# Optimization experiments

Measured on AMD Instinct MI355X. Metric: run time of the kernel, lower is better.

The kernel has to match this reference:

```python
import jax, jax.numpy as jnp
import numpy as np

B, S, VOCAB, E, H, T = 256, 512, 50000, 256, 256, 32
PAD = VOCAB - 1  # mask = sentences != vocab_size - 1 in the original


def setup_inputs() -> dict:
    key = jax.random.key(0)
    ks = jax.random.split(key, 16)
    lengths = jnp.sort(jax.random.randint(ks[0], (B,), S // 2, S + 1))[::-1]
    lengths = lengths.at[0].set(S)  # sorted descending, max length present
    sentences = jax.random.randint(ks[1], (B, S), 0, VOCAB - 1)
    pos = jnp.arange(S)
    sentences = jnp.where(pos[None, :] < lengths[:, None], sentences, PAD)
    tags = jax.random.randint(ks[2], (B, S), 0, T)
    sc = jnp.float32(0.1)
    p = lambda k, shp: jax.random.normal(k, shp, jnp.float32) * sc
    return {
        'embed_table': p(ks[3], (VOCAB + 1, E)),
        'W_ih_f': p(ks[4], (4 * H, E)), 'W_hh_f': p(ks[5], (4 * H, H)),
        'b_ih_f': p(ks[6], (4 * H,)), 'b_hh_f': p(ks[7], (4 * H,)),
        'W_ih_b': p(ks[8], (4 * H, E)), 'W_hh_b': p(ks[9], (4 * H, H)),
        'b_ih_b': p(ks[10], (4 * H,)), 'b_hh_b': p(ks[11], (4 * H,)),
        'W_out': p(ks[12], (T, 2 * H)), 'b_out': p(ks[13], (T,)),
        'transition': jax.random.normal(ks[14], (T, T), jnp.float32),
        'sentences': sentences, 'tags': tags, 'sen_lengths': lengths,
    }


def _run_lstm(x_sbe, W_ih, W_hh, b_ih, b_hh):
    # x_sbe: [S, B, E]; torch gate order i, f, g, o
    Bsz, Hd = x_sbe.shape[1], W_hh.shape[1]
    gx = jnp.einsum('sbe,ge->sbg', x_sbe, W_ih) + b_ih + b_hh  # precompute input gates
    def step(carry, g):
        h, c = carry
        g = g + h @ W_hh.T
        i, f, gg, o = jnp.split(g, 4, axis=-1)
        c = jax.nn.sigmoid(f) * c + jax.nn.sigmoid(i) * jnp.tanh(gg)
        h = jax.nn.sigmoid(o) * jnp.tanh(c)
        return (h, c), h
    h0 = jnp.zeros((Bsz, Hd), x_sbe.dtype)
    _, hs = jax.lax.scan(step, (h0, h0), gx)
    return hs  # [S, B, H]


def _forward(embed_table, W_ih_f, W_hh_f, b_ih_f, b_hh_f,
             W_ih_b, W_hh_b, b_ih_b, b_hh_b, W_out, b_out, transition,
             sentences, tags, sen_lengths):
    mask = sentences != PAD                      # [B, S]
    x = embed_table[sentences]                   # [B, S, E]
    pos = jnp.arange(S)
    valid = pos[None, :] < sen_lengths[:, None]  # [B, S]
    # per-sequence reversal index (packed-sequence-faithful backward direction)
    idx = jnp.where(valid, sen_lengths[:, None] - 1 - pos[None, :], pos[None, :])
    h_f = _run_lstm(x.transpose(1, 0, 2), W_ih_f, W_hh_f, b_ih_f, b_hh_f).transpose(1, 0, 2)
    x_rev = jnp.take_along_axis(x, idx[:, :, None], axis=1)
    h_b = _run_lstm(x_rev.transpose(1, 0, 2), W_ih_b, W_hh_b, b_ih_b, b_hh_b).transpose(1, 0, 2)
    h_b = jnp.take_along_axis(h_b, idx[:, :, None], axis=1)
    h = jnp.concatenate([h_f, h_b], -1) * valid[:, :, None]  # pad_packed pads with zeros
    emit = h @ W_out.T + b_out                   # [B, S, T]; dropout is identity (eval)
    # ---- CRF negative log-likelihood ----
    fmask = mask.astype(emit.dtype)
    real = jnp.take_along_axis(emit, tags[:, :, None], axis=2)[..., 0]  # [B, S]
    real = real.at[:, 1:].add(transition[tags[:, :-1], tags[:, 1:]])
    real_score = (real * fmask).sum(axis=1)      # [B]
    def crf_step(alpha, inp):
        e_i, m_i = inp                           # [B, T], [B]
        scores = alpha[:, :, None] + transition[None, :, :] + e_i[:, None, :]
        new = jax.nn.logsumexp(scores, axis=1)
        return jnp.where(m_i[:, None], new, alpha), None
    alpha0 = emit[:, 0]                          # [B, T]
    xs = (emit[:, 1:].transpose(1, 0, 2), mask[:, 1:].T)
    alpha, _ = jax.lax.scan(crf_step, alpha0, xs)
    log_z = jax.nn.logsumexp(alpha, axis=1)      # [B]
    return -(real_score - log_z)                 # per-example loss [B]


def reference(embed_table, W_ih_f, W_hh_f, b_ih_f, b_hh_f,
              W_ih_b, W_hh_b, b_ih_b, b_hh_b, W_out, b_out, transition,
              sentences, tags, sen_lengths):
    return _forward(embed_table, W_ih_f, W_hh_f, b_ih_f, b_hh_f,
                    W_ih_b, W_hh_b, b_ih_b, b_hh_b, W_out, b_out, transition,
                    sentences, tags, sen_lengths)
```

## Files before the change

kernel.cpp:

```cpp
#include <hip/hip_runtime.h>
#include <hip/hip_bf16.h>


typedef __bf16 bf16x8 __attribute__((ext_vector_type(8)));
typedef float f32x4 __attribute__((ext_vector_type(4)));
typedef unsigned int uint4v __attribute__((ext_vector_type(4)));

__device__ __forceinline__ unsigned short f2bf(float f) {
  union { float f; unsigned int u; } v; v.f = f;
  unsigned int r = v.u + 0x7fffu + ((v.u >> 16) & 1u);
  return (unsigned short)(r >> 16);
}
__device__ __forceinline__ float bf2f(unsigned int lo16) {
  union { unsigned int u; float f; } v; v.u = lo16 << 16;
  return v.f;
}
__device__ __forceinline__ float fsig(float x) {
  float e = __builtin_amdgcn_exp2f(-1.4426950408889634f * x);
  return __builtin_amdgcn_rcpf(1.0f + e);
}
__device__ __forceinline__ float ftanh(float x) {
  float e = __builtin_amdgcn_exp2f(2.8853900817779268f * x);
  return 1.0f - 2.0f * __builtin_amdgcn_rcpf(e + 1.0f);
}

__global__ void cvt_weights(const float* __restrict__ wih_f, const float* __restrict__ wih_b,
                            const float* __restrict__ whh_f, const float* __restrict__ whh_b,
                            const float* __restrict__ wo,
                            unsigned short* __restrict__ wih,
                            unsigned char* __restrict__ whh8,
                            unsigned char* __restrict__ wout8) {
  int t = blockIdx.x * 256 + threadIdx.x;
  int i = t * 4;
  if (i < 524288) {
    const float* src = (i < 262144) ? wih_f : wih_b;
    f32x4 v = *(const f32x4*)(src + (i & 262143));
    uint2 p;
    p.x = f2bf(v[0]) | ((unsigned int)f2bf(v[1]) << 16);
    p.y = f2bf(v[2]) | ((unsigned int)f2bf(v[3]) << 16);
    *(uint2*)(wih + i) = p;
  } else if (i < 1048576) {
    int k = i - 524288;
    const float* src = (k < 262144) ? whh_f : whh_b;
    f32x4 v = *(const f32x4*)(src + (k & 262143));
    int r = 0;
    r = __builtin_amdgcn_cvt_pk_fp8_f32(v[0], v[1], r, false);
    r = __builtin_amdgcn_cvt_pk_fp8_f32(v[2], v[3], r, true);
    *(unsigned int*)(whh8 + k) = (unsigned int)r;
  } else if (i < 1064960) {
    int k = i - 1048576;
    f32x4 v = *(const f32x4*)(wo + k);
    int r = 0;
    r = __builtin_amdgcn_cvt_pk_fp8_f32(v[0], v[1], r, false);
    r = __builtin_amdgcn_cvt_pk_fp8_f32(v[2], v[3], r, true);
    *(unsigned int*)(wout8 + k) = (unsigned int)r;
  }
}


__device__ __forceinline__ void gemm_role(
    const float* __restrict__ emb, const int* __restrict__ sent, const int* __restrict__ lens,
    const unsigned short* __restrict__ wih,
    const float* __restrict__ bih_f, const float* __restrict__ bhh_f,
    const float* __restrict__ bih_b, const float* __restrict__ bhh_b,
    unsigned short* __restrict__ gx, int k,
    unsigned short* wtile, float* btile)
{
  int g = blockIdx.x - 64;
  int dir = g >> 7, r = g & 127;
  int nc = r >> 4, bt = (r >> 2) & 3, ss = r & 3;
  int n0 = nc * 128, bbase = bt * 64;
  int s0 = k * 32;
  int sbase = s0 + ss * 8;
  if (sbase >= lens[bbase]) return;
  int p = k & 1;
  int tid = threadIdx.x, w = tid >> 6, lane = tid & 63, col = lane & 15, q = lane >> 4;
  int ns = w >> 2, cg = w & 3;

  const unsigned short* wsrc = wih + (size_t)dir * 262144;
#pragma unroll
  for (int it = 0; it < 8; it++) {
    int seg = it * 512 + tid;
    int row = seg >> 5, kc = (seg & 31) * 8;
    *(uint4v*)(wtile + row * 264 + kc) = *(const uint4v*)(wsrc + (size_t)(n0 + row) * 256 + kc);
  }
  const float* bi = dir ? bih_b : bih_f;
  const float* bh = dir ? bhh_b : bhh_f;
  if (tid < 128) btile[tid] = bi[n0 + tid] + bh[n0 + tid];
  __syncthreads();

  bf16x8 wf[8][4];
#pragma unroll
  for (int kt = 0; kt < 8; kt++)
#pragma unroll
    for (int nt = 0; nt < 4; nt++)
      wf[kt][nt] = *(const bf16x8*)(wtile + (ns * 64 + nt * 16 + col) * 264 + kt * 32 + q * 8);
  f32x4 bias[4];
#pragma unroll
  for (int nt = 0; nt < 4; nt++)
#pragma unroll
    for (int rr = 0; rr < 4; rr++)
      bias[nt][rr] = btile[ns * 64 + nt * 16 + q * 4 + rr];

  int bidx = bbase + cg * 16 + col;
  int len = lens[bidx];
  const int* srow = sent + bidx * 512;

  for (int i = 0; i < 8; i++) {
    int s = sbase + i;
    int s_eff = dir ? ((s < len) ? (len - 1 - s) : s) : s;
    int token = srow[s_eff];
    const float* ep = emb + (size_t)token * 256;
    bf16x8 xf[8];
#pragma unroll
    for (int kt = 0; kt < 8; kt++) {
      f32x4 a0 = *(const f32x4*)(ep + kt * 32 + q * 8);
      f32x4 a1 = *(const f32x4*)(ep + kt * 32 + q * 8 + 4);
      uint4v pk;
      pk[0] = f2bf(a0[0]) | ((unsigned int)f2bf(a0[1]) << 16);
      pk[1] = f2bf(a0[2]) | ((unsigned int)f2bf(a0[3]) << 16);
      pk[2] = f2bf(a1[0]) | ((unsigned int)f2bf(a1[1]) << 16);
      pk[3] = f2bf(a1[2]) | ((unsigned int)f2bf(a1[3]) << 16);
      xf[kt] = __builtin_bit_cast(bf16x8, pk);
    }
    f32x4 acc[4];
#pragma unroll
    for (int nt = 0; nt < 4; nt++) acc[nt] = bias[nt];
#pragma unroll
    for (int kt = 0; kt < 8; kt++)
#pragma unroll
      for (int nt = 0; nt < 4; nt++)
        acc[nt] = __builtin_amdgcn_mfma_f32_16x16x32_bf16(wf[kt][nt], xf[kt], acc[nt], 0, 0, 0);
    size_t off = (size_t)p * 16777216 + (size_t)dir * 8388608
               + (size_t)(s - s0) * 262144 + (size_t)bidx * 1024 + n0 + ns * 64;
#pragma unroll
    for (int nt = 0; nt < 4; nt++) {
      uint2 pk;
      pk.x = f2bf(acc[nt][0]) | ((unsigned int)f2bf(acc[nt][1]) << 16);
      pk.y = f2bf(acc[nt][2]) | ((unsigned int)f2bf(acc[nt][3]) << 16);
      *(uint2*)(gx + off + nt * 16 + q * 4) = pk;
    }
  }
}

__device__ __forceinline__ void lstm_role(
    const unsigned short* __restrict__ gx,
    const unsigned char* __restrict__ whh8,
    const unsigned char* __restrict__ wout8,
    const float* __restrict__ bout,
    const int* __restrict__ lens,
    unsigned short* __restrict__ emit_f, unsigned short* __restrict__ emit_b,
    unsigned short* __restrict__ h_state, float* __restrict__ c_state,
    int k, unsigned char (*hbuf)[16 * 264])
{
  int cl = k - 1;
  int s0 = cl * 32, first = (cl == 0), p = cl & 1;
  int bx = blockIdx.x;
  int dir = bx & 1, grp = bx >> 1, b0 = grp * 8;
  int tid = threadIdx.x, w = tid >> 6, lane = tid & 63, col = lane & 15, q = lane >> 4;
  int maxlen = lens[b0];
  if (s0 >= maxlen) return;
  int send = s0 + 32; if (send > maxlen) send = maxlen;
  int bcl = b0 + col; if (bcl > 255) bcl = 255;
  int mylen = lens[bcl];

  const unsigned char* whb = whh8 + (size_t)dir * 262144;
  long wh[8][8];
#pragma unroll
  for (int kt = 0; kt < 8; kt++)
#pragma unroll
    for (int t = 0; t < 8; t++) {
      int row0 = (t & 3) * 256 + w * 32 + (t >> 2) * 16;
      wh[kt][t] = *(const long*)(whb + (size_t)(row0 + col) * 256 + kt * 32 + q * 8);
    }

  long wo8[8];
  f32x4 bo4 = (f32x4){0.f, 0.f, 0.f, 0.f};
  if (w < 2) {
#pragma unroll
    for (int kt = 0; kt < 8; kt++)
      wo8[kt] = *(const long*)(wout8 + (size_t)(w * 16 + col) * 512 + dir * 256 + kt * 32 + q * 8);
    if (dir == 0) {
#pragma unroll
      for (int r = 0; r < 4; r++) bo4[r] = bout[w * 16 + q * 4 + r];
    }
  }
  unsigned short* ebase = dir ? emit_b : emit_f;

  size_t stoff = ((size_t)bx * 16 + col) * 256 + w * 32;
  float c8[8];
  long hf8[8];
  if (first) {
#pragma unroll
    for (int i = 0; i < 8; i++) c8[i] = 0.f;
#pragma unroll
    for (int i = 0; i < 8; i++) hf8[i] = 0;
  } else {
    int pf = (s0 + 1) & 1;
#pragma unroll
    for (int a = 0; a < 2; a++) {
      f32x4 cv = *(const f32x4*)(c_state + stoff + a * 16 + q * 4);
#pragma unroll
      for (int r = 0; r < 4; r++) c8[a * 4 + r] = cv[r];
      uint2 hb = *(const uint2*)(h_state + stoff + a * 16 + q * 4);
      float h0 = bf2f(hb.x & 0xffffu), h1 = bf2f(hb.x >> 16);
      float h2 = bf2f(hb.y & 0xffffu), h3 = bf2f(hb.y >> 16);
      int r8 = 0;
      r8 = __builtin_amdgcn_cvt_pk_fp8_f32(h0, h1, r8, false);
      r8 = __builtin_amdgcn_cvt_pk_fp8_f32(h2, h3, r8, true);
      *(unsigned int*)(&hbuf[pf][col * 264 + w * 32 + a * 16 + q * 4]) = (unsigned int)r8;
    }
    __syncthreads();
#pragma unroll
    for (int kt = 0; kt < 8; kt++)
      hf8[kt] = *(const long*)(&hbuf[pf][col * 264 + kt * 32 + q * 8]);
  }

  const unsigned short* gl = gx + (size_t)p * 16777216 + (size_t)dir * 8388608
                                + (size_t)bcl * 1024 + q * 4;
  uint2 gxr[8];
#pragma unroll
  for (int t = 0; t < 8; t++) {
    int row0 = (t & 3) * 256 + w * 32 + (t >> 2) * 16;
    gxr[t] = *(const uint2*)(gl + row0);
  }

  for (int s = s0; s < send; s++) {
    f32x4 acc[8];
#pragma unroll
    for (int t = 0; t < 8; t++) {
      f32x4 a;
      a[0] = bf2f(gxr[t].x & 0xffffu); a[1] = bf2f(gxr[t].x >> 16);
      a[2] = bf2f(gxr[t].y & 0xffffu); a[3] = bf2f(gxr[t].y >> 16);
      acc[t] = a;
    }
    {
      int snl = (s + 1 < send) ? (s + 1 - s0) : (send - 1 - s0);
      const unsigned short* gn = gl + (size_t)snl * 262144;
#pragma unroll
      for (int t = 0; t < 8; t++) {
        int row0 = (t & 3) * 256 + w * 32 + (t >> 2) * 16;
        gxr[t] = *(const uint2*)(gn + row0);
      }
    }
#pragma unroll
    for (int kt = 0; kt < 8; kt++) {
      long hv8 = hf8[kt];
#pragma unroll
      for (int t = 0; t < 8; t++)
        acc[t] = __builtin_amdgcn_mfma_f32_16x16x32_fp8_fp8(wh[kt][t], hv8, acc[t], 0, 0, 0);
    }
    float hv[8];
#pragma unroll
    for (int a = 0; a < 2; a++)
#pragma unroll
      for (int r = 0; r < 4; r++) {
        float ig = acc[a * 4 + 0][r], fg = acc[a * 4 + 1][r];
        float gg = acc[a * 4 + 2][r], og = acc[a * 4 + 3][r];
        float cn = fsig(fg) * c8[a * 4 + r] + fsig(ig) * ftanh(gg);
        c8[a * 4 + r] = cn;
        hv[a * 4 + r] = fsig(og) * ftanh(cn);
      }
    int par = s & 1;
#pragma unroll
    for (int a = 0; a < 2; a++) {
      int r8 = 0;
      r8 = __builtin_amdgcn_cvt_pk_fp8_f32(hv[a * 4 + 0], hv[a * 4 + 1], r8, false);
      r8 = __builtin_amdgcn_cvt_pk_fp8_f32(hv[a * 4 + 2], hv[a * 4 + 3], r8, true);
      *(unsigned int*)(&hbuf[par][col * 264 + w * 32 + a * 16 + q * 4]) = (unsigned int)r8;
    }
    if (s == send - 1) {
#pragma unroll
      for (int a = 0; a < 2; a++) {
        uint2 pp;
        pp.x = f2bf(hv[a * 4 + 0]) | ((unsigned int)f2bf(hv[a * 4 + 1]) << 16);
        pp.y = f2bf(hv[a * 4 + 2]) | ((unsigned int)f2bf(hv[a * 4 + 3]) << 16);
        *(uint2*)(h_state + stoff + a * 16 + q * 4) = pp;
      }
    }
    __syncthreads();
#pragma unroll
    for (int kt = 0; kt < 8; kt++)
      hf8[kt] = *(const long*)(&hbuf[par][col * 264 + kt * 32 + q * 8]);

    if (w < 2) {
      f32x4 ea = bo4;
#pragma unroll
      for (int kt = 0; kt < 8; kt++)
        ea = __builtin_amdgcn_mfma_f32_16x16x32_fp8_fp8(wo8[kt], hf8[kt], ea, 0, 0, 0);
      if (col < 8 && s < mylen) {
        int pos = dir ? (mylen - 1 - s) : s;
        uint2 pk;
        pk.x = f2bf(ea[0]) | ((unsigned int)f2bf(ea[1]) << 16);
        pk.y = f2bf(ea[2]) | ((unsigned int)f2bf(ea[3]) << 16);
        *(uint2*)(ebase + (((size_t)(b0 + col) * 512 + pos) * 32 + w * 16 + q * 4)) = pk;
      }
    }
  }
#pragma unroll
  for (int a = 0; a < 2; a++) {
    f32x4 cv;
#pragma unroll
    for (int r = 0; r < 4; r++) cv[r] = c8[a * 4 + r];
    *(f32x4*)(c_state + stoff + a * 16 + q * 4) = cv;
  }
}

__global__ __launch_bounds__(512, 2) void fused_step(
    const float* __restrict__ emb, const int* __restrict__ sent, const int* __restrict__ lens,
    const unsigned short* __restrict__ wih,
    const float* __restrict__ bih_f, const float* __restrict__ bhh_f,
    const float* __restrict__ bih_b, const float* __restrict__ bhh_b,
    unsigned short* __restrict__ gx,
    const unsigned char* __restrict__ whh8, const unsigned char* __restrict__ wout8,
    const float* __restrict__ bout,
    unsigned short* __restrict__ emit_f, unsigned short* __restrict__ emit_b,
    unsigned short* __restrict__ h_state, float* __restrict__ c_state,
    int k)
{
  __shared__ __align__(16) unsigned short wtile[128 * 264];
  __shared__ __align__(16) float btile[128];
  __shared__ __align__(16) unsigned char hbuf[2][16 * 264];

  if (blockIdx.x < 64) {
    if (k == 0) return;
    lstm_role(gx, whh8, wout8, bout, lens, emit_f, emit_b, h_state, c_state, k, hbuf);
  } else {
    if (k == 16) return;
    gemm_role(emb, sent, lens, wih, bih_f, bhh_f, bih_b, bhh_b, gx, k, wtile, btile);
  }
}

__global__ __launch_bounds__(64) void crf_kernel(
    const unsigned short* __restrict__ emit_f,
    const unsigned short* __restrict__ emit_b,
    const float* __restrict__ trans, const int* __restrict__ tags,
    const int* __restrict__ lens, float* __restrict__ out) {
  const float LOG2E = 1.4426950408889634f, LN2 = 0.6931471805599453f;
  __shared__ __align__(16) float e_lds[512 * 32];
  int b = blockIdx.x, lane = threadIdx.x;
  int len = lens[b];
  const int* tg = tags + b * 512;

  size_t ebase = (size_t)b * 512 * 32;
  const unsigned short* pf = emit_f + ebase;
  const unsigned short* pb = emit_b + ebase;
  int ng = len * 4;
  for (int g = lane; g < ng; g += 64) {
    uint4v fv = *(const uint4v*)(pf + g * 8);
    uint4v bv = *(const uint4v*)(pb + g * 8);
    f32x4 w0, w1;
#pragma unroll
    for (int k = 0; k < 2; k++) {
      w0[2 * k]     = (bf2f(fv[k] & 0xffffu) + bf2f(bv[k] & 0xffffu)) * LOG2E;
      w0[2 * k + 1] = (bf2f(fv[k] >> 16)     + bf2f(bv[k] >> 16))     * LOG2E;
      w1[2 * k]     = (bf2f(fv[k + 2] & 0xffffu) + bf2f(bv[k + 2] & 0xffffu)) * LOG2E;
      w1[2 * k + 1] = (bf2f(fv[k + 2] >> 16)     + bf2f(bv[k + 2] >> 16))     * LOG2E;
    }
    *(f32x4*)(e_lds + g * 8) = w0;
    *(f32x4*)(e_lds + g * 8 + 4) = w1;
  }
  __syncthreads();

  float rs2 = 0.f, rst = 0.f;
  for (int s = lane; s < len; s += 64) {
    int t1 = tg[s];
    rs2 += e_lds[s * 32 + t1];
    if (s > 0) rst += trans[tg[s - 1] * 32 + t1];
  }
  float rsc = LN2 * rs2 + rst;
#pragma unroll
  for (int m = 32; m; m >>= 1) rsc += __shfl_xor(rsc, m);

  int j = lane & 31, half = lane >> 5, i0 = half * 16;
  float tr2[16];
  int pidx[16];
#pragma unroll
  for (int ii = 0; ii < 16; ii++) {
    tr2[ii] = trans[(i0 + ii) * 32 + j] * LOG2E;
    pidx[ii] = (i0 + ii) << 2;
  }
  const float* ep = e_lds + j;
  float B = ep[0];
  float e_nxt = ep[32];
  for (int s = 1; s < len; s++) {
    float e_cur = e_nxt;
    int sn = (s + 1 < len) ? (s + 1) : s;
    e_nxt = ep[sn * 32];
    float v[16];
#pragma unroll
    for (int ii = 0; ii < 16; ii++)
      v[ii] = __builtin_bit_cast(float, __builtin_amdgcn_ds_bpermute(
                  pidx[ii], __builtin_bit_cast(int, B))) + tr2[ii];
    float a8[8], a4[4], a2[2];
#pragma unroll
    for (int ii = 0; ii < 8; ii++) a8[ii] = fmaxf(v[ii], v[ii + 8]);
#pragma unroll
    for (int ii = 0; ii < 4; ii++) a4[ii] = fmaxf(a8[ii], a8[ii + 4]);
    a2[0] = fmaxf(a4[0], a4[2]); a2[1] = fmaxf(a4[1], a4[3]);
    float m1 = fmaxf(a2[0], a2[1]);
    float m2 = fmaxf(m1, __shfl_xor(m1, 32));
    float x[16];
#pragma unroll
    for (int ii = 0; ii < 16; ii++) x[ii] = __builtin_amdgcn_exp2f(v[ii] - m2);
    float s8[8], s4[4], s2[2];
#pragma unroll
    for (int ii = 0; ii < 8; ii++) s8[ii] = x[ii] + x[ii + 8];
#pragma unroll
    for (int ii = 0; ii < 4; ii++) s4[ii] = s8[ii] + s8[ii + 4];
    s2[0] = s4[0] + s4[2]; s2[1] = s4[1] + s4[3];
    float sum = s2[0] + s2[1];
    sum += __shfl_xor(sum, 32);
    B = m2 + __builtin_amdgcn_logf(sum) + e_cur;
  }
  float mz = B;
#pragma unroll
  for (int m = 16; m; m >>= 1) mz = fmaxf(mz, __shfl_xor(mz, m));
  float sz = __builtin_amdgcn_exp2f(B - mz);
#pragma unroll
  for (int m = 16; m; m >>= 1) sz += __shfl_xor(sz, m);
  float logz = LN2 * (mz + __builtin_amdgcn_logf(sz));
  if (lane == 0) out[b] = logz - rsc;
}

extern "C" void kernel_launch(void* const* d_in, const int* in_sizes, int n_in,
                              void* d_out, int out_size, void* d_ws, size_t ws_size,
                              hipStream_t stream) {
  const float* emb   = (const float*)d_in[0];
  const float* Wih_f = (const float*)d_in[1];
  const float* Whh_f = (const float*)d_in[2];
  const float* bih_f = (const float*)d_in[3];
  const float* bhh_f = (const float*)d_in[4];
  const float* Wih_b = (const float*)d_in[5];
  const float* Whh_b = (const float*)d_in[6];
  const float* bih_b = (const float*)d_in[7];
  const float* bhh_b = (const float*)d_in[8];
  const float* Wout  = (const float*)d_in[9];
  const float* bout  = (const float*)d_in[10];
  const float* trans = (const float*)d_in[11];
  const int* sent = (const int*)d_in[12];
  const int* tags = (const int*)d_in[13];
  const int* lens = (const int*)d_in[14];
  float* out = (float*)d_out;

  char* ws = (char*)d_ws;
  if (ws_size < 87048192ull) return;
  unsigned short* gx      = (unsigned short*)(ws);
  unsigned short* emit_f  = (unsigned short*)(ws + 67108864);
  unsigned short* emit_b  = (unsigned short*)(ws + 75497472);
  unsigned short* wih_bf  = (unsigned short*)(ws + 83886080);
  unsigned char*  whh8    = (unsigned char*)(ws + 84934656);
  unsigned char*  wout8   = (unsigned char*)(ws + 85458944);
  unsigned short* h_state = (unsigned short*)(ws + 85475328);
  float*          c_state = (float*)(ws + 85999616);

  cvt_weights<<<1040, 256, 0, stream>>>(Wih_f, Wih_b, Whh_f, Whh_b, Wout,
                                        wih_bf, whh8, wout8);
  for (int k = 0; k <= 16; k++) {
    fused_step<<<320, 512, 0, stream>>>(
        emb, sent, lens, wih_bf, bih_f, bhh_f, bih_b, bhh_b, gx,
        whh8, wout8, bout, emit_f, emit_b, h_state, c_state, k);
  }
  crf_kernel<<<256, 64, 0, stream>>>(emit_f, emit_b, trans, tags, lens, out);
}
```

Baseline: 1.665 ms.

## Replace per-chunk kernel launches with a persistent kernel using atomic flag handoff

Replaces the 17 sequential launches of the fused step with one persistent kernel. Its 64 LSTM blocks keep h and c in registers across all chunks, and 192 GEMM blocks loop over chunk tiles. Producer and consumer synchronise through release/acquire atomic counters in global memory. This removes per-launch overhead and the h/c state spill to global memory between chunks. It also lets the input-gate GEMM run ahead of the recurrence, limited by the double-buffered gx. The output projection is now batched every 4 steps from an 8-deep LDS h ring, using all warps. This adds a dependence on all 256 blocks being co-resident, otherwise the spin-waits could deadlock.

```diff
diff --git a/kernel.cpp b/kernel.cpp
--- a/kernel.cpp
+++ b/kernel.cpp
@@ -22,6 +22,15 @@
 __device__ __forceinline__ float ftanh(float x) {
   float e = __builtin_amdgcn_exp2f(2.8853900817779268f * x);
   return 1.0f - 2.0f * __builtin_amdgcn_rcpf(e + 1.0f);
+}
+
+__device__ __forceinline__ void wait_ge(int* p, int target) {
+  if (threadIdx.x == 0) {
+    while (__hip_atomic_load(p, __ATOMIC_RELAXED, __HIP_MEMORY_SCOPE_AGENT) < target)
+      __builtin_amdgcn_s_sleep(2);
+    (void)__hip_atomic_load(p, __ATOMIC_ACQUIRE, __HIP_MEMORY_SCOPE_AGENT);
+  }
+  __syncthreads();
 }
 
 __global__ void cvt_weights(const float* __restrict__ wih_f, const float* __restrict__ wih_b,
@@ -29,7 +38,9 @@
                             const float* __restrict__ wo,
                             unsigned short* __restrict__ wih,
                             unsigned char* __restrict__ whh8,
-                            unsigned char* __restrict__ wout8) {
+                            unsigned char* __restrict__ wout8,
+                            int* __restrict__ flags) {
+  if (blockIdx.x == 0 && threadIdx.x < 32) flags[threadIdx.x] = 0;
   int t = blockIdx.x * 256 + threadIdx.x;
   int i = t * 4;
   if (i < 524288) {
@@ -58,109 +69,115 @@
 }
 
 
-__device__ __forceinline__ void gemm_role(
+__device__ void gemm_role(
     const float* __restrict__ emb, const int* __restrict__ sent, const int* __restrict__ lens,
     const unsigned short* __restrict__ wih,
     const float* __restrict__ bih_f, const float* __restrict__ bhh_f,
     const float* __restrict__ bih_b, const float* __restrict__ bhh_b,
-    unsigned short* __restrict__ gx, int k,
+    unsigned short* __restrict__ gx, int* flags,
     unsigned short* wtile, float* btile)
 {
-  int g = blockIdx.x - 64;
-  int dir = g >> 7, r = g & 127;
-  int nc = r >> 4, bt = (r >> 2) & 3, ss = r & 3;
-  int n0 = nc * 128, bbase = bt * 64;
-  int s0 = k * 32;
-  int sbase = s0 + ss * 8;
-  if (sbase >= lens[bbase]) return;
-  int p = k & 1;
+  int gb = blockIdx.x - 64;
   int tid = threadIdx.x, w = tid >> 6, lane = tid & 63, col = lane & 15, q = lane >> 4;
   int ns = w >> 2, cg = w & 3;
-
-  const unsigned short* wsrc = wih + (size_t)dir * 262144;
-#pragma unroll
-  for (int it = 0; it < 8; it++) {
-    int seg = it * 512 + tid;
-    int row = seg >> 5, kc = (seg & 31) * 8;
-    *(uint4v*)(wtile + row * 264 + kc) = *(const uint4v*)(wsrc + (size_t)(n0 + row) * 256 + kc);
-  }
-  const float* bi = dir ? bih_b : bih_f;
-  const float* bh = dir ? bhh_b : bhh_f;
-  if (tid < 128) btile[tid] = bi[n0 + tid] + bh[n0 + tid];
-  __syncthreads();
-
-  bf16x8 wf[8][4];
-#pragma unroll
-  for (int kt = 0; kt < 8; kt++)
-#pragma unroll
-    for (int nt = 0; nt < 4; nt++)
-      wf[kt][nt] = *(const bf16x8*)(wtile + (ns * 64 + nt * 16 + col) * 264 + kt * 32 + q * 8);
-  f32x4 bias[4];
-#pragma unroll
-  for (int nt = 0; nt < 4; nt++)
-#pragma unroll
-    for (int rr = 0; rr < 4; rr++)
-      bias[nt][rr] = btile[ns * 64 + nt * 16 + q * 4 + rr];
-
-  int bidx = bbase + cg * 16 + col;
-  int len = lens[bidx];
-  const int* srow = sent + bidx * 512;
-
-  for (int i = 0; i < 8; i++) {
-    int s = sbase + i;
-    int s_eff = dir ? ((s < len) ? (len - 1 - s) : s) : s;
-    int token = srow[s_eff];
-    const float* ep = emb + (size_t)token * 256;
-    bf16x8 xf[8];
-#pragma unroll
-    for (int kt = 0; kt < 8; kt++) {
-      f32x4 a0 = *(const f32x4*)(ep + kt * 32 + q * 8);
-      f32x4 a1 = *(const f32x4*)(ep + kt * 32 + q * 8 + 4);
-      uint4v pk;
-      pk[0] = f2bf(a0[0]) | ((unsigned int)f2bf(a0[1]) << 16);
-      pk[1] = f2bf(a0[2]) | ((unsigned int)f2bf(a0[3]) << 16);
-      pk[2] = f2bf(a1[0]) | ((unsigned int)f2bf(a1[1]) << 16);
-      pk[3] = f2bf(a1[2]) | ((unsigned int)f2bf(a1[3]) << 16);
-      xf[kt] = __builtin_bit_cast(bf16x8, pk);
+  int prev_chunk = -1;
+
+  for (int idx = gb; idx < 4096; idx += 192) {
+    int k = idx >> 8, t = idx & 255;
+    if (k != prev_chunk) {
+      prev_chunk = k;
+      if (k >= 2) wait_ge(&flags[16 + k - 2], 64);
     }
-    f32x4 acc[4];
-#pragma unroll
-    for (int nt = 0; nt < 4; nt++) acc[nt] = bias[nt];
-#pragma unroll
-    for (int kt = 0; kt < 8; kt++)
+    int dir = t >> 7, r = t & 127;
+    int nc = r >> 4, bt = (r >> 2) & 3, ss = r & 3;
+    int n0 = nc * 128, bbase = bt * 64;
+    int s0 = k * 32, sbase = s0 + ss * 8;
+
+    if (sbase < lens[bbase]) {
+      const unsigned short* wsrc = wih + (size_t)dir * 262144;
+#pragma unroll
+      for (int it = 0; it < 8; it++) {
+        int seg = it * 512 + tid;
+        int row = seg >> 5, kc = (seg & 31) * 8;
+        *(uint4v*)(wtile + row * 264 + kc) = *(const uint4v*)(wsrc + (size_t)(n0 + row) * 256 + kc);
+      }
+      const float* bi = dir ? bih_b : bih_f;
+      const float* bh = dir ? bhh_b : bhh_f;
+      if (tid < 128) btile[tid] = bi[n0 + tid] + bh[n0 + tid];
+      __syncthreads();
+
+      bf16x8 wf[8][4];
+#pragma unroll
+      for (int kt = 0; kt < 8; kt++)
+#pragma unroll
+        for (int nt = 0; nt < 4; nt++)
+          wf[kt][nt] = *(const bf16x8*)(wtile + (ns * 64 + nt * 16 + col) * 264 + kt * 32 + q * 8);
+      f32x4 bias[4];
 #pragma unroll
       for (int nt = 0; nt < 4; nt++)
-        acc[nt] = __builtin_amdgcn_mfma_f32_16x16x32_bf16(wf[kt][nt], xf[kt], acc[nt], 0, 0, 0);
-    size_t off = (size_t)p * 16777216 + (size_t)dir * 8388608
-               + (size_t)(s - s0) * 262144 + (size_t)bidx * 1024 + n0 + ns * 64;
-#pragma unroll
-    for (int nt = 0; nt < 4; nt++) {
-      uint2 pk;
-      pk.x = f2bf(acc[nt][0]) | ((unsigned int)f2bf(acc[nt][1]) << 16);
-      pk.y = f2bf(acc[nt][2]) | ((unsigned int)f2bf(acc[nt][3]) << 16);
-      *(uint2*)(gx + off + nt * 16 + q * 4) = pk;
+#pragma unroll
+        for (int rr = 0; rr < 4; rr++)
+          bias[nt][rr] = btile[ns * 64 + nt * 16 + q * 4 + rr];
+
+      int bidx = bbase + cg * 16 + col;
+      int len = lens[bidx];
+      const int* srow = sent + bidx * 512;
+
+      for (int i = 0; i < 8; i++) {
+        int s = sbase + i;
+        int s_eff = dir ? ((s < len) ? (len - 1 - s) : s) : s;
+        int token = srow[s_eff];
+        const float* ep = emb + (size_t)token * 256;
+        bf16x8 xf[8];
+#pragma unroll
+        for (int kt = 0; kt < 8; kt++) {
+          f32x4 a0 = *(const f32x4*)(ep + kt * 32 + q * 8);
+          f32x4 a1 = *(const f32x4*)(ep + kt * 32 + q * 8 + 4);
+          uint4v pk;
+          pk[0] = f2bf(a0[0]) | ((unsigned int)f2bf(a0[1]) << 16);
+          pk[1] = f2bf(a0[2]) | ((unsigned int)f2bf(a0[3]) << 16);
+          pk[2] = f2bf(a1[0]) | ((unsigned int)f2bf(a1[1]) << 16);
+          pk[3] = f2bf(a1[2]) | ((unsigned int)f2bf(a1[3]) << 16);
+          xf[kt] = __builtin_bit_cast(bf16x8, pk);
+        }
+        f32x4 acc[4];
+#pragma unroll
+        for (int nt = 0; nt < 4; nt++) acc[nt] = bias[nt];
+#pragma unroll
+        for (int kt = 0; kt < 8; kt++)
+#pragma unroll
+          for (int nt = 0; nt < 4; nt++)
+            acc[nt] = __builtin_amdgcn_mfma_f32_16x16x32_bf16(wf[kt][nt], xf[kt], acc[nt], 0, 0, 0);
+        size_t off = (size_t)(k & 1) * 16777216 + (size_t)dir * 8388608
+                   + (size_t)(s - s0) * 262144 + (size_t)bidx * 1024 + n0 + ns * 64;
+#pragma unroll
+        for (int nt = 0; nt < 4; nt++) {
+          uint2 pk;
+          pk.x = f2bf(acc[nt][0]) | ((unsigned int)f2bf(acc[nt][1]) << 16);
+          pk.y = f2bf(acc[nt][2]) | ((unsigned int)f2bf(acc[nt][3]) << 16);
+          *(uint2*)(gx + off + nt * 16 + q * 4) = pk;
+        }
+      }
     }
-  }
-}
-
-__device__ __forceinline__ void lstm_role(
+    __syncthreads();
+    if (tid == 0)
+      __hip_atomic_fetch_add(&flags[k], 1, __ATOMIC_RELEASE, __HIP_MEMORY_SCOPE_AGENT);
+  }
+}
+
+__device__ void lstm_role(
     const unsigned short* __restrict__ gx,
     const unsigned char* __restrict__ whh8,
     const unsigned char* __restrict__ wout8,
     const float* __restrict__ bout,
     const int* __restrict__ lens,
     unsigned short* __restrict__ emit_f, unsigned short* __restrict__ emit_b,
-    unsigned short* __restrict__ h_state, float* __restrict__ c_state,
-    int k, unsigned char (*hbuf)[16 * 264])
+    int* flags, unsigned char (*hb4)[16 * 264])
 {
-  int cl = k - 1;
-  int s0 = cl * 32, first = (cl == 0), p = cl & 1;
   int bx = blockIdx.x;
   int dir = bx & 1, grp = bx >> 1, b0 = grp * 8;
   int tid = threadIdx.x, w = tid >> 6, lane = tid & 63, col = lane & 15, q = lane >> 4;
   int maxlen = lens[b0];
-  if (s0 >= maxlen) return;
-  int send = s0 + 32; if (send > maxlen) send = maxlen;
   int bcl = b0 + col; if (bcl > 255) bcl = 255;
   int mylen = lens[bcl];
 
@@ -176,137 +193,111 @@
 
   long wo8[8];
   f32x4 bo4 = (f32x4){0.f, 0.f, 0.f, 0.f};
-  if (w < 2) {
-#pragma unroll
-    for (int kt = 0; kt < 8; kt++)
-      wo8[kt] = *(const long*)(wout8 + (size_t)(w * 16 + col) * 512 + dir * 256 + kt * 32 + q * 8);
-    if (dir == 0) {
-#pragma unroll
-      for (int r = 0; r < 4; r++) bo4[r] = bout[w * 16 + q * 4 + r];
-    }
+#pragma unroll
+  for (int kt = 0; kt < 8; kt++)
+    wo8[kt] = *(const long*)(wout8 + (size_t)((w & 1) * 16 + col) * 512 + dir * 256 + kt * 32 + q * 8);
+  if (dir == 0) {
+#pragma unroll
+    for (int r = 0; r < 4; r++) bo4[r] = bout[(w & 1) * 16 + q * 4 + r];
   }
   unsigned short* ebase = dir ? emit_b : emit_f;
 
-  size_t stoff = ((size_t)bx * 16 + col) * 256 + w * 32;
   float c8[8];
   long hf8[8];
-  if (first) {
-#pragma unroll
-    for (int i = 0; i < 8; i++) c8[i] = 0.f;
-#pragma unroll
-    for (int i = 0; i < 8; i++) hf8[i] = 0;
-  } else {
-    int pf = (s0 + 1) & 1;
-#pragma unroll
-    for (int a = 0; a < 2; a++) {
-      f32x4 cv = *(const f32x4*)(c_state + stoff + a * 16 + q * 4);
-#pragma unroll
-      for (int r = 0; r < 4; r++) c8[a * 4 + r] = cv[r];
-      uint2 hb = *(const uint2*)(h_state + stoff + a * 16 + q * 4);
-      float h0 = bf2f(hb.x & 0xffffu), h1 = bf2f(hb.x >> 16);
-      float h2 = bf2f(hb.y & 0xffffu), h3 = bf2f(hb.y >> 16);
-      int r8 = 0;
-      r8 = __builtin_amdgcn_cvt_pk_fp8_f32(h0, h1, r8, false);
-      r8 = __builtin_amdgcn_cvt_pk_fp8_f32(h2, h3, r8, true);
-      *(unsigned int*)(&hbuf[pf][col * 264 + w * 32 + a * 16 + q * 4]) = (unsigned int)r8;
-    }
-    __syncthreads();
-#pragma unroll
-    for (int kt = 0; kt < 8; kt++)
-      hf8[kt] = *(const long*)(&hbuf[pf][col * 264 + kt * 32 + q * 8]);
-  }
-
-  const unsigned short* gl = gx + (size_t)p * 16777216 + (size_t)dir * 8388608
-                                + (size_t)bcl * 1024 + q * 4;
-  uint2 gxr[8];
-#pragma unroll
-  for (int t = 0; t < 8; t++) {
-    int row0 = (t & 3) * 256 + w * 32 + (t >> 2) * 16;
-    gxr[t] = *(const uint2*)(gl + row0);
-  }
-
-  for (int s = s0; s < send; s++) {
-    f32x4 acc[8];
-#pragma unroll
-    for (int t = 0; t < 8; t++) {
-      f32x4 a;
-      a[0] = bf2f(gxr[t].x & 0xffffu); a[1] = bf2f(gxr[t].x >> 16);
-      a[2] = bf2f(gxr[t].y & 0xffffu); a[3] = bf2f(gxr[t].y >> 16);
-      acc[t] = a;
-    }
-    {
-      int snl = (s + 1 < send) ? (s + 1 - s0) : (send - 1 - s0);
-      const unsigned short* gn = gl + (size_t)snl * 262144;
+#pragma unroll
+  for (int i = 0; i < 8; i++) { c8[i] = 0.f; hf8[i] = 0; }
+
+  for (int c = 0; c < 16; c++) {
+    int s0 = c * 32;
+    if (s0 < maxlen) {
+      wait_ge(&flags[c], 256);
+      int send = s0 + 32; if (send > maxlen) send = maxlen;
+      const unsigned short* gl = gx + (size_t)(c & 1) * 16777216 + (size_t)dir * 8388608
+                                    + (size_t)bcl * 1024 + q * 4;
+      uint2 gxr[8];
 #pragma unroll
       for (int t = 0; t < 8; t++) {
         int row0 = (t & 3) * 256 + w * 32 + (t >> 2) * 16;
-        gxr[t] = *(const uint2*)(gn + row0);
+        gxr[t] = *(const uint2*)(gl + row0);
       }
-    }
-#pragma unroll
-    for (int kt = 0; kt < 8; kt++) {
-      long hv8 = hf8[kt];
-#pragma unroll
-      for (int t = 0; t < 8; t++)
-        acc[t] = __builtin_amdgcn_mfma_f32_16x16x32_fp8_fp8(wh[kt][t], hv8, acc[t], 0, 0, 0);
-    }
-    float hv[8];
-#pragma unroll
-    for (int a = 0; a < 2; a++)
-#pragma unroll
-      for (int r = 0; r < 4; r++) {
-        float ig = acc[a * 4 + 0][r], fg = acc[a * 4 + 1][r];
-        float gg = acc[a * 4 + 2][r], og = acc[a * 4 + 3][r];
-        float cn = fsig(fg) * c8[a * 4 + r] + fsig(ig) * ftanh(gg);
-        c8[a * 4 + r] = cn;
-        hv[a * 4 + r] = fsig(og) * ftanh(cn);
-      }
-    int par = s & 1;
-#pragma unroll
-    for (int a = 0; a < 2; a++) {
-      int r8 = 0;
-      r8 = __builtin_amdgcn_cvt_pk_fp8_f32(hv[a * 4 + 0], hv[a * 4 + 1], r8, false);
-      r8 = __builtin_amdgcn_cvt_pk_fp8_f32(hv[a * 4 + 2], hv[a * 4 + 3], r8, true);
-      *(unsigned int*)(&hbuf[par][col * 264 + w * 32 + a * 16 + q * 4]) = (unsigned int)r8;
-    }
-    if (s == send - 1) {
-#pragma unroll
-      for (int a = 0; a < 2; a++) {
-        uint2 pp;
-        pp.x = f2bf(hv[a * 4 + 0]) | ((unsigned int)f2bf(hv[a * 4 + 1]) << 16);
-        pp.y = f2bf(hv[a * 4 + 2]) | ((unsigned int)f2bf(hv[a * 4 + 3]) << 16);
-        *(uint2*)(h_state + stoff + a * 16 + q * 4) = pp;
+
+      for (int s = s0; s < send; s++) {
+        f32x4 acc[8];
+#pragma unroll
+        for (int t = 0; t < 8; t++) {
+          f32x4 a;
+          a[0] = bf2f(gxr[t].x & 0xffffu); a[1] = bf2f(gxr[t].x >> 16);
+          a[2] = bf2f(gxr[t].y & 0xffffu); a[3] = bf2f(gxr[t].y >> 16);
+          acc[t] = a;
+        }
+        {
+          int snl = (s + 1 < send) ? (s + 1 - s0) : (send - 1 - s0);
+          const unsigned short* gn = gl + (size_t)snl * 262144;
+#pragma unroll
+          for (int t = 0; t < 8; t++) {
+            int row0 = (t & 3) * 256 + w * 32 + (t >> 2) * 16;
+            gxr[t] = *(const uint2*)(gn + row0);
+          }
+        }
+#pragma unroll
+        for (int kt = 0; kt < 8; kt++) {
+          long hv8 = hf8[kt];
+#pragma unroll
+          for (int t = 0; t < 8; t++)
+            acc[t] = __builtin_amdgcn_mfma_f32_16x16x32_fp8_fp8(wh[kt][t], hv8, acc[t], 0, 0, 0);
+        }
+        float hv[8];
+#pragma unroll
+        for (int a = 0; a < 2; a++)
+#pragma unroll
+          for (int r = 0; r < 4; r++) {
+            float ig = acc[a * 4 + 0][r], fg = acc[a * 4 + 1][r];
+            float gg = acc[a * 4 + 2][r], og = acc[a * 4 + 3][r];
+            float cn = fsig(fg) * c8[a * 4 + r] + fsig(ig) * ftanh(gg);
+            c8[a * 4 + r] = cn;
+            hv[a * 4 + r] = fsig(og) * ftanh(cn);
+          }
+        int par = s & 7;
+#pragma unroll
+        for (int a = 0; a < 2; a++) {
+          int r8 = 0;
+          r8 = __builtin_amdgcn_cvt_pk_fp8_f32(hv[a * 4 + 0], hv[a * 4 + 1], r8, false);
+          r8 = __builtin_amdgcn_cvt_pk_fp8_f32(hv[a * 4 + 2], hv[a * 4 + 3], r8, true);
+          *(unsigned int*)(&hb4[par][col * 264 + w * 32 + a * 16 + q * 4]) = (unsigned int)r8;
+        }
+        __syncthreads();
+#pragma unroll
+        for (int kt = 0; kt < 8; kt++)
+          hf8[kt] = *(const long*)(&hb4[par][col * 264 + kt * 32 + q * 8]);
+
+        if ((s & 3) == 3 || s == send - 1) {
+          int ebeg = s & ~3;
+          int e = ebeg + (w >> 1);
+          if (e <= s) {
+            f32x4 ea = bo4;
+#pragma unroll
+            for (int kt = 0; kt < 8; kt++) {
+              long hbv = *(const long*)(&hb4[e & 7][col * 264 + kt * 32 + q * 8]);
+              ea = __builtin_amdgcn_mfma_f32_16x16x32_fp8_fp8(wo8[kt], hbv, ea, 0, 0, 0);
+            }
+            if (col < 8 && e < mylen) {
+              int pos = dir ? (mylen - 1 - e) : e;
+              uint2 pk;
+              pk.x = f2bf(ea[0]) | ((unsigned int)f2bf(ea[1]) << 16);
+              pk.y = f2bf(ea[2]) | ((unsigned int)f2bf(ea[3]) << 16);
+              *(uint2*)(ebase + (((size_t)(b0 + col) * 512 + pos) * 32 + (w & 1) * 16 + q * 4)) = pk;
+            }
+          }
+        }
       }
     }
     __syncthreads();
-#pragma unroll
-    for (int kt = 0; kt < 8; kt++)
-      hf8[kt] = *(const long*)(&hbuf[par][col * 264 + kt * 32 + q * 8]);
-
-    if (w < 2) {
-      f32x4 ea = bo4;
-#pragma unroll
-      for (int kt = 0; kt < 8; kt++)
-        ea = __builtin_amdgcn_mfma_f32_16x16x32_fp8_fp8(wo8[kt], hf8[kt], ea, 0, 0, 0);
-      if (col < 8 && s < mylen) {
-        int pos = dir ? (mylen - 1 - s) : s;
-        uint2 pk;
-        pk.x = f2bf(ea[0]) | ((unsigned int)f2bf(ea[1]) << 16);
-        pk.y = f2bf(ea[2]) | ((unsigned int)f2bf(ea[3]) << 16);
-        *(uint2*)(ebase + (((size_t)(b0 + col) * 512 + pos) * 32 + w * 16 + q * 4)) = pk;
-      }
-    }
-  }
-#pragma unroll
-  for (int a = 0; a < 2; a++) {
-    f32x4 cv;
-#pragma unroll
-    for (int r = 0; r < 4; r++) cv[r] = c8[a * 4 + r];
-    *(f32x4*)(c_state + stoff + a * 16 + q * 4) = cv;
-  }
-}
-
-__global__ __launch_bounds__(512, 2) void fused_step(
+    if (tid == 0)
+      __hip_atomic_fetch_add(&flags[16 + c], 1, __ATOMIC_RELEASE, __HIP_MEMORY_SCOPE_AGENT);
+  }
+}
+
+__global__ __launch_bounds__(512, 2) void fused_persist(
     const float* __restrict__ emb, const int* __restrict__ sent, const int* __restrict__ lens,
     const unsigned short* __restrict__ wih,
     const float* __restrict__ bih_f, const float* __restrict__ bhh_f,
@@ -315,19 +306,16 @@
     const unsigned char* __restrict__ whh8, const unsigned char* __restrict__ wout8,
     const float* __restrict__ bout,
     unsigned short* __restrict__ emit_f, unsigned short* __restrict__ emit_b,
-    unsigned short* __restrict__ h_state, float* __restrict__ c_state,
-    int k)
+    int* flags)
 {
   __shared__ __align__(16) unsigned short wtile[128 * 264];
   __shared__ __align__(16) float btile[128];
-  __shared__ __align__(16) unsigned char hbuf[2][16 * 264];
+  __shared__ __align__(16) unsigned char hb4[8][16 * 264];
 
   if (blockIdx.x < 64) {
-    if (k == 0) return;
-    lstm_role(gx, whh8, wout8, bout, lens, emit_f, emit_b, h_state, c_state, k, hbuf);
+    lstm_role(gx, whh8, wout8, bout, lens, emit_f, emit_b, flags, hb4);
   } else {
-    if (k == 16) return;
-    gemm_role(emb, sent, lens, wih, bih_f, bhh_f, bih_b, bhh_b, gx, k, wtile, btile);
+    gemm_role(emb, sent, lens, wih, bih_f, bhh_f, bih_b, bhh_b, gx, flags, wtile, btile);
   }
 }
 
@@ -451,15 +439,12 @@
   unsigned short* wih_bf  = (unsigned short*)(ws + 83886080);
   unsigned char*  whh8    = (unsigned char*)(ws + 84934656);
   unsigned char*  wout8   = (unsigned char*)(ws + 85458944);
-  unsigned short* h_state = (unsigned short*)(ws + 85475328);
-  float*          c_state = (float*)(ws + 85999616);
+  int*            flags   = (int*)(ws + 85475328);
 
   cvt_weights<<<1040, 256, 0, stream>>>(Wih_f, Wih_b, Whh_f, Whh_b, Wout,
-                                        wih_bf, whh8, wout8);
-  for (int k = 0; k <= 16; k++) {
-    fused_step<<<320, 512, 0, stream>>>(
-        emb, sent, lens, wih_bf, bih_f, bhh_f, bih_b, bhh_b, gx,
-        whh8, wout8, bout, emit_f, emit_b, h_state, c_state, k);
-  }
+                                        wih_bf, whh8, wout8, flags);
+  fused_persist<<<256, 512, 0, stream>>>(
+      emb, sent, lens, wih_bf, bih_f, bhh_f, bih_b, bhh_b, gx,
+      whh8, wout8, bout, emit_f, emit_b, flags);
   crf_kernel<<<256, 64, 0, stream>>>(emit_f, emit_b, trans, tags, lens, out);
 }
```

Measured after the change: 1.735 ms. 1.04x slower.
